# Optimization experiments

Hardware: AMD Instinct MI355X
Metric: run time of the kernel (lower is better)

Reference implementation:

```python
import jax, jax.numpy as jnp
import numpy as np

KNOW = 128
EXER_N = 20000
STU_N = 50000
N_EDGES = 1000000
N_EDGES_P = 950000
BATCH = 8192
SOFT_PARA = 0.2
EPS = 1e-8


def setup_inputs() -> dict:
    key = jax.random.key(0)
    ks = jax.random.split(key, 10)
    return {
        'stu_emb': jax.random.normal(ks[0], (STU_N, KNOW), jnp.float32) * 0.1,
        'exer_emb': jax.random.normal(ks[1], (EXER_N, KNOW), jnp.float32) * 0.1,
        'W_ue': jax.random.normal(ks[2], (KNOW, KNOW), jnp.float32) / np.sqrt(KNOW),
        'W_ue_per': jax.random.normal(ks[3], (KNOW, KNOW), jnp.float32) / np.sqrt(KNOW),
        'W_deep': jax.random.normal(ks[4], (KNOW, KNOW), jnp.float32) / np.sqrt(KNOW),
        'src_e': jax.random.randint(ks[5], (N_EDGES,), 0, EXER_N),
        'dst_e': jax.random.randint(ks[6], (N_EDGES,), 0, STU_N),
        'src_p': jax.random.randint(ks[7], (N_EDGES_P,), 0, EXER_N),
        'dst_p': jax.random.randint(ks[8], (N_EDGES_P,), 0, STU_N),
        'stu_id': jax.random.randint(ks[9], (BATCH,), 0, STU_N),
    }


def _graph_layer(exer, W, src, dst):
    # u_from_e: messages flow exercise -> student. Linear transform then mean-aggregate.
    msg = exer[src] @ W                                   # [E_edges, K]
    agg = jax.ops.segment_sum(msg, dst, num_segments=STU_N)
    deg = jax.ops.segment_sum(jnp.ones_like(dst, jnp.float32), dst, num_segments=STU_N)
    return agg / jnp.maximum(deg, 1.0)[:, None]           # [STU_N, K]


def reference(stu_emb, exer_emb, W_ue, W_ue_per, W_deep, src_e, dst_e, src_p, dst_p, stu_id):
    # ExpressionDooubleEva: two parallel graph views
    stu1 = stu_emb + _graph_layer(exer_emb, W_ue, src_e, dst_e)
    stu_per = stu_emb + _graph_layer(exer_emb, W_ue_per, src_p, dst_p)
    # ExpressionSingleEva (u_from_e output is overwritten by u_from_e_deep in source)
    stu2 = stu1 + _graph_layer(exer_emb, W_deep, src_e, dst_e)
    stu2_per = stu_per + _graph_layer(exer_emb, W_deep, src_e, dst_e)

    b1 = stu2[stu_id]          # [B, K]
    b2 = stu2_per[stu_id]      # [B, K]
    n1 = b1 / jnp.linalg.norm(b1, axis=1, keepdims=True)
    n2 = b2 / jnp.linalg.norm(b2, axis=1, keepdims=True)
    sim = (n1 @ n2.T) / SOFT_PARA                         # [B, B]
    # faithful to source: numerator = exp(diag(sim)), denominator = sum of RAW sim row
    diag_exp = jnp.exp(jnp.diagonal(sim))
    row_sum = jnp.sum(sim, axis=1)
    ratio = diag_exp / (row_sum + EPS)
    ssl_loss = jnp.mean(-jnp.log(jnp.maximum(ratio, EPS)))
    return stu2, ssl_loss
```

## Files before the change

kernel.cpp:

```cpp
#include <hip/hip_runtime.h>
#include <math.h>

#define KNOW 128
#define STU_N 50000
#define EXER_N 20000
#define BATCH 8192
#define NE 1000000
#define NEP 950000
#define SOFT_INV 5.0f
#define EPS 1e-8f

#define CAP 64
#define NBIN 256
#define SPB 196
#define SSE 4608
#define SSP 1536
#define P1B 256
#define P1T 512
#define SFB 32
#define WPB 24
#define TFB 250
#define BM_T 80

typedef unsigned short u16;
typedef unsigned int u32;

typedef __attribute__((ext_vector_type(8))) short bf16x8;
typedef __attribute__((ext_vector_type(4))) float f32x4;

__device__ __forceinline__ u16 f2bf(float f) {
  union { float f; u32 u; } v;
  v.f = f;
  u32 r = (v.u + 0x7FFFu + ((v.u >> 16) & 1u)) >> 16;
  return (u16)r;
}
__device__ __forceinline__ float bflo(u32 u) {
  union { u32 u; float f; } v;
  v.u = u << 16;
  return v.f;
}
__device__ __forceinline__ float bfhi(u32 u) {
  union { u32 u; float f; } v;
  v.u = u & 0xFFFF0000u;
  return v.f;
}
__device__ __forceinline__ float bfu(u16 h) {
  union { u32 u; float f; } v;
  v.u = ((u32)h) << 16;
  return v.f;
}

#define ADD8(A, q)            \
  {                           \
    A[0] += bflo((q).x);      \
    A[1] += bfhi((q).x);      \
    A[2] += bflo((q).y);      \
    A[3] += bfhi((q).y);      \
    A[4] += bflo((q).z);      \
    A[5] += bfhi((q).z);      \
    A[6] += bflo((q).w);      \
    A[7] += bfhi((q).w);      \
  }

__global__ __launch_bounds__(256) void prep_flags(
    const int* __restrict__ stu_id, unsigned char* __restrict__ flag,
    int* __restrict__ gcur_e, int* __restrict__ gcur_p,
    const float* __restrict__ exer, const float* __restrict__ W_ue,
    const float* __restrict__ W_per, const float* __restrict__ W_deep,
    u16* __restrict__ Ah, u16* __restrict__ Al, u16* __restrict__ WTh,
    u16* __restrict__ WTl) {
  int b = blockIdx.x;
  int t = threadIdx.x;
  if (b < SFB) {
    int i = b * 256 + t;
    if (i < BATCH) flag[stu_id[i]] = 1;
    if (i < NBIN) {
      gcur_e[i] = i * SSE;
      gcur_p[i] = i * SSP;
    }
  } else if (b < SFB + WPB) {
    int plane = (b - SFB) >> 3;
    int slab = (b - SFB) & 7;
    int n = t & 127;
    int k0 = slab * 16 + (t >> 7) * 8;
    const float* W0 = (plane == 0) ? W_ue : (plane == 1) ? W_per : W_deep;
    float x[8];
#pragma unroll
    for (int j = 0; j < 8; ++j) {
      float v = W0[(k0 + j) * KNOW + n];
      if (plane == 0) v += W_deep[(k0 + j) * KNOW + n];
      x[j] = v;
    }
    u16 hi[8], lo[8];
#pragma unroll
    for (int j = 0; j < 8; ++j) {
      u16 h = f2bf(x[j]);
      hi[j] = h;
      lo[j] = f2bf(x[j] - bfu(h));
    }
    size_t base = ((size_t)plane * KNOW + n) * KNOW + k0;
    uint4 H = {(u32)hi[0] | ((u32)hi[1] << 16), (u32)hi[2] | ((u32)hi[3] << 16),
               (u32)hi[4] | ((u32)hi[5] << 16), (u32)hi[6] | ((u32)hi[7] << 16)};
    uint4 L = {(u32)lo[0] | ((u32)lo[1] << 16), (u32)lo[2] | ((u32)lo[3] << 16),
               (u32)lo[4] | ((u32)lo[5] << 16), (u32)lo[6] | ((u32)lo[7] << 16)};
    *(uint4*)(WTh + base) = H;
    *(uint4*)(WTl + base) = L;
  } else {
    size_t i = ((size_t)(b - SFB - WPB) * 256 + t) * 4;
    float4 v = *(const float4*)(exer + i);
    u16 h0 = f2bf(v.x), h1 = f2bf(v.y), h2 = f2bf(v.z), h3 = f2bf(v.w);
    ushort4 H = {h0, h1, h2, h3};
    ushort4 L = {f2bf(v.x - bfu(h0)), f2bf(v.y - bfu(h1)), f2bf(v.z - bfu(h2)),
                 f2bf(v.w - bfu(h3))};
    *(ushort4*)(Ah + i) = H;
    *(ushort4*)(Al + i) = L;
  }
}

__global__ __launch_bounds__(P1T) void transform_bin1(
    const u16* __restrict__ Ah, const u16* __restrict__ Al,
    const u16* __restrict__ WTh, const u16* __restrict__ WTl,
    u16* __restrict__ X_sum, u16* __restrict__ X_per,
    u16* __restrict__ X_deep, const int* __restrict__ dst_e,
    const int* __restrict__ src_e, const int* __restrict__ dst_p,
    const int* __restrict__ src_p, const unsigned char* __restrict__ flag,
    int* __restrict__ gcur_e, int* __restrict__ gcur_p,
    u32* __restrict__ stag_e, u32* __restrict__ stag_p) {
  __shared__ int cntE[NBIN], cntP[NBIN];
  __shared__ int baseE[NBIN], baseP[NBIN];
  __shared__ int curE[NBIN], curP[NBIN];
  int t = threadIdx.x;
  if (blockIdx.x < P1B) {
    if (t < NBIN) {
      cntE[t] = 0;
      cntP[t] = 0;
    }
    __syncthreads();
    int b = blockIdx.x;
    int e0 = (int)((long long)NE * b / P1B);
    int e1 = (int)((long long)NE * (b + 1) / P1B);
    int p0 = (int)((long long)NEP * b / P1B);
    int p1 = (int)((long long)NEP * (b + 1) / P1B);
    for (int i = e0 + t; i < e1; i += P1T) {
      int d = __builtin_nontemporal_load(&dst_e[i]);
      atomicAdd(&cntE[d / SPB], 1);
    }
    for (int i = p0 + t; i < p1; i += P1T) {
      int d = __builtin_nontemporal_load(&dst_p[i]);
      if (flag[d]) atomicAdd(&cntP[d / SPB], 1);
    }
    __syncthreads();
    if (t < NBIN) {
      baseE[t] = atomicAdd(&gcur_e[t], cntE[t]);
      baseP[t] = atomicAdd(&gcur_p[t], cntP[t]);
      curE[t] = 0;
      curP[t] = 0;
    }
    __syncthreads();
    for (int i = e0 + t; i < e1; i += P1T) {
      int d = __builtin_nontemporal_load(&dst_e[i]);
      int s = __builtin_nontemporal_load(&src_e[i]);
      int bin = d / SPB;
      int pos = baseE[bin] + atomicAdd(&curE[bin], 1);
      if (pos < (bin + 1) * SSE)
        stag_e[pos] = ((u32)(d - bin * SPB) << 16) | (u32)s;
    }
    for (int i = p0 + t; i < p1; i += P1T) {
      int d = __builtin_nontemporal_load(&dst_p[i]);
      if (!flag[d]) continue;
      int s = __builtin_nontemporal_load(&src_p[i]);
      int bin = d / SPB;
      int pos = baseP[bin] + atomicAdd(&curP[bin], 1);
      if (pos < (bin + 1) * SSP)
        stag_p[pos] = ((u32)(d - bin * SPB) << 16) | (u32)s;
    }
  } else {
    int wv = t >> 6;
    int l = t & 63;
    int bn = l & 15;
    int kb = l >> 4;
    int row0 = (blockIdx.x - P1B) * BM_T;
    int n = wv * 16 + bn;
#pragma unroll 1
    for (int which = 0; which < 3; ++which) {
      u16* outp = (which == 0) ? X_sum : (which == 1) ? X_per : X_deep;
      const u16* wth = WTh + (size_t)which * KNOW * KNOW;
      const u16* wtl = WTl + (size_t)which * KNOW * KNOW;
      bf16x8 bh[4], bl[4];
#pragma unroll
      for (int ks = 0; ks < 4; ++ks) {
        int off = n * KNOW + ks * 32 + kb * 8;
        bh[ks] = *(const bf16x8*)(wth + off);
        bl[ks] = *(const bf16x8*)(wtl + off);
      }
#pragma unroll 1
      for (int rt = 0; rt < 5; ++rt) {
        int row = row0 + rt * 16 + bn;
        const u16* ap = Ah + (size_t)row * KNOW + kb * 8;
        const u16* alp = Al + (size_t)row * KNOW + kb * 8;
        f32x4 acc = {0.f, 0.f, 0.f, 0.f};
#pragma unroll
        for (int ks = 0; ks < 4; ++ks) {
          bf16x8 af = *(const bf16x8*)(ap + ks * 32);
          bf16x8 lf = *(const bf16x8*)(alp + ks * 32);
          acc = __builtin_amdgcn_mfma_f32_16x16x32_bf16(af, bh[ks], acc, 0, 0, 0);
          acc = __builtin_amdgcn_mfma_f32_16x16x32_bf16(lf, bh[ks], acc, 0, 0, 0);
          acc = __builtin_amdgcn_mfma_f32_16x16x32_bf16(af, bl[ks], acc, 0, 0, 0);
        }
        int orow = row0 + rt * 16 + kb * 4;
#pragma unroll
        for (int r = 0; r < 4; ++r)
          outp[(size_t)(orow + r) * KNOW + n] = f2bf(acc[r]);
      }
    }
  }
}

__global__ __launch_bounds__(256) void bin_pass2(
    const u32* __restrict__ stag_e, const u32* __restrict__ stag_p,
    const int* __restrict__ gcur_e, const int* __restrict__ gcur_p,
    u16* __restrict__ bucket_e, u16* __restrict__ bucket_p,
    int* __restrict__ cnt_e, int* __restrict__ cnt_p) {
  __shared__ u16 be[SPB * CAP];
  __shared__ u16 bp[SPB * CAP];
  __shared__ int ce[SPB], cp[SPB];
  int t = threadIdx.x;
  int bin = blockIdx.x;
  for (int i = t; i < SPB; i += 256) {
    ce[i] = 0;
    cp[i] = 0;
  }
  __syncthreads();
  int ne = gcur_e[bin] - bin * SSE;
  if (ne > SSE) ne = SSE;
  int np = gcur_p[bin] - bin * SSP;
  if (np > SSP) np = SSP;
  const u32* se = stag_e + (size_t)bin * SSE;
  for (int i = t; i < ne; i += 256) {
    u32 w = se[i];
    int dl = (int)(w >> 16), s = (int)(w & 0xFFFFu);
    int slot = atomicAdd(&ce[dl], 1);
    if (slot < CAP) be[dl * CAP + slot] = (u16)s;
  }
  const u32* sp = stag_p + (size_t)bin * SSP;
  for (int i = t; i < np; i += 256) {
    u32 w = sp[i];
    int dl = (int)(w >> 16), s = (int)(w & 0xFFFFu);
    int slot = atomicAdd(&cp[dl], 1);
    if (slot < CAP) bp[dl * CAP + slot] = (u16)s;
  }
  __syncthreads();
  int s0 = bin * SPB;
  int nstu = STU_N - s0;
  if (nstu > SPB) nstu = SPB;
  if (nstu <= 0) return;
  int nvec = nstu * CAP * 2 / 16;
  const uint4* bev = (const uint4*)be;
  uint4* ge = (uint4*)(bucket_e + (size_t)s0 * CAP);
  for (int i = t; i < nvec; i += 256) ge[i] = bev[i];
  const uint4* bpv = (const uint4*)bp;
  uint4* gp = (uint4*)(bucket_p + (size_t)s0 * CAP);
  for (int i = t; i < nvec; i += 256) gp[i] = bpv[i];
  for (int i = t; i < nstu; i += 256) {
    cnt_e[s0 + i] = ce[i];
    cnt_p[s0 + i] = cp[i];
  }
}

__global__ __launch_bounds__(256) void stu2_gather(
    const float* __restrict__ stu_emb, const u16* __restrict__ X_sum,
    const u16* __restrict__ bucket, const int* __restrict__ cnt,
    float* __restrict__ out) {
  int wv = threadIdx.x >> 6;
  int l = threadIdx.x & 63;
  int s = blockIdx.x * 4 + wv;
  if (s >= STU_N) return;
  int deg = cnt[s];
  int e = (deg < CAP) ? deg : CAP;
  u32 bval = bucket[(size_t)s * CAP + l];
  int g = l >> 4;
  int c = l & 15;
  float acc[8] = {};
  for (int i = g; i < e; i += 16) {
    int iB = i + 4, iC = i + 8, iD = i + 12;
    int jB = (iB < e) ? iB : i;
    int jC = (iC < e) ? iC : i;
    int jD = (iD < e) ? iD : i;
    int rA = __shfl((int)bval, i);
    int rB = __shfl((int)bval, jB);
    int rC = __shfl((int)bval, jC);
    int rD = __shfl((int)bval, jD);
    const uint4 qA = *(const uint4*)(X_sum + (size_t)rA * KNOW + c * 8);
    const uint4 qB = *(const uint4*)(X_sum + (size_t)rB * KNOW + c * 8);
    const uint4 qC = *(const uint4*)(X_sum + (size_t)rC * KNOW + c * 8);
    const uint4 qD = *(const uint4*)(X_sum + (size_t)rD * KNOW + c * 8);
    ADD8(acc, qA);
    if (iB < e) ADD8(acc, qB);
    if (iC < e) ADD8(acc, qC);
    if (iD < e) ADD8(acc, qD);
  }
#pragma unroll
  for (int j = 0; j < 8; ++j) {
    float v = acc[j];
    v += __shfl_xor(v, 16);
    v += __shfl_xor(v, 32);
    acc[j] = v;
  }
  if (l < 16) {
    float inv = 1.0f / fmaxf((float)deg, 1.0f);
    float4 se0 = *(const float4*)(stu_emb + (size_t)s * KNOW + c * 8);
    float4 se1 = *(const float4*)(stu_emb + (size_t)s * KNOW + c * 8 + 4);
    float4 o0 = {se0.x + acc[0] * inv, se0.y + acc[1] * inv,
                 se0.z + acc[2] * inv, se0.w + acc[3] * inv};
    float4 o1 = {se1.x + acc[4] * inv, se1.y + acc[5] * inv,
                 se1.z + acc[6] * inv, se1.w + acc[7] * inv};
    *(float4*)(out + (size_t)s * KNOW + c * 8) = o0;
    *(float4*)(out + (size_t)s * KNOW + c * 8 + 4) = o1;
  }
}

__global__ __launch_bounds__(256) void batch_kernel(
    const float* __restrict__ stu_emb, const float* __restrict__ stu2,
    const u16* __restrict__ X_per, const u16* __restrict__ X_deep,
    const u16* __restrict__ bucket_p, const int* __restrict__ cnt_p,
    const u16* __restrict__ bucket_e, const int* __restrict__ cnt_e,
    const int* __restrict__ stu_id, float* __restrict__ n1,
    float* __restrict__ n2, float* __restrict__ diag) {
  int wv = threadIdx.x >> 6;
  int l = threadIdx.x & 63;
  int i = blockIdx.x * 4 + wv;
  int sid = stu_id[i];
  int g = l >> 4;
  int c = l & 15;

  int degp = cnt_p[sid];
  int degd = cnt_e[sid];
  u32 bvp = bucket_p[(size_t)sid * CAP + l];
  u32 bvd = bucket_e[(size_t)sid * CAP + l];
  int ep = (degp < CAP) ? degp : CAP;
  int ed = (degd < CAP) ? degd : CAP;

  float ap[8] = {};
  for (int t = g; t < ep; t += 16) {
    int iB = t + 4, iC = t + 8, iD = t + 12;
    int jB = (iB < ep) ? iB : t;
    int jC = (iC < ep) ? iC : t;
    int jD = (iD < ep) ? iD : t;
    int rA = __shfl((int)bvp, t);
    int rB = __shfl((int)bvp, jB);
    int rC = __shfl((int)bvp, jC);
    int rD = __shfl((int)bvp, jD);
    const uint4 qA = *(const uint4*)(X_per + (size_t)rA * KNOW + c * 8);
    const uint4 qB = *(const uint4*)(X_per + (size_t)rB * KNOW + c * 8);
    const uint4 qC = *(const uint4*)(X_per + (size_t)rC * KNOW + c * 8);
    const uint4 qD = *(const uint4*)(X_per + (size_t)rD * KNOW + c * 8);
    ADD8(ap, qA);
    if (iB < ep) ADD8(ap, qB);
    if (iC < ep) ADD8(ap, qC);
    if (iD < ep) ADD8(ap, qD);
  }

  float ad[8] = {};
  for (int t = g; t < ed; t += 16) {
    int iB = t + 4, iC = t + 8, iD = t + 12;
    int jB = (iB < ed) ? iB : t;
    int jC = (iC < ed) ? iC : t;
    int jD = (iD < ed) ? iD : t;
    int rA = __shfl((int)bvd, t);
    int rB = __shfl((int)bvd, jB);
    int rC = __shfl((int)bvd, jC);
    int rD = __shfl((int)bvd, jD);
    const uint4 qA = *(const uint4*)(X_deep + (size_t)rA * KNOW + c * 8);
    const uint4 qB = *(const uint4*)(X_deep + (size_t)rB * KNOW + c * 8);
    const uint4 qC = *(const uint4*)(X_deep + (size_t)rC * KNOW + c * 8);
    const uint4 qD = *(const uint4*)(X_deep + (size_t)rD * KNOW + c * 8);
    ADD8(ad, qA);
    if (iB < ed) ADD8(ad, qB);
    if (iC < ed) ADD8(ad, qC);
    if (iD < ed) ADD8(ad, qD);
  }

#pragma unroll
  for (int j = 0; j < 8; ++j) {
    float v = ap[j];
    v += __shfl_xor(v, 16);
    v += __shfl_xor(v, 32);
    ap[j] = v;
    float w = ad[j];
    w += __shfl_xor(w, 16);
    w += __shfl_xor(w, 32);
    ad[j] = w;
  }

  float invp = 1.0f / fmaxf((float)degp, 1.0f);
  float invd = 1.0f / fmaxf((float)degd, 1.0f);
  float4 e0 = *(const float4*)(stu_emb + (size_t)sid * KNOW + c * 8);
  float4 e1 = *(const float4*)(stu_emb + (size_t)sid * KNOW + c * 8 + 4);
  float4 s0 = *(const float4*)(stu2 + (size_t)sid * KNOW + c * 8);
  float4 s1 = *(const float4*)(stu2 + (size_t)sid * KNOW + c * 8 + 4);
  float b1v[8] = {s0.x, s0.y, s0.z, s0.w, s1.x, s1.y, s1.z, s1.w};
  float ev[8] = {e0.x, e0.y, e0.z, e0.w, e1.x, e1.y, e1.z, e1.w};
  float b2v[8];
  float s11 = 0.f, s22 = 0.f, s12 = 0.f;
#pragma unroll
  for (int j = 0; j < 8; ++j) {
    b2v[j] = ev[j] + ap[j] * invp + ad[j] * invd;
    s11 += b1v[j] * b1v[j];
    s22 += b2v[j] * b2v[j];
    s12 += b1v[j] * b2v[j];
  }
#pragma unroll
  for (int off = 1; off <= 8; off <<= 1) {
    s11 += __shfl_xor(s11, off);
    s22 += __shfl_xor(s22, off);
    s12 += __shfl_xor(s12, off);
  }
  float norm1 = sqrtf(s11);
  float norm2 = sqrtf(s22);
  if (g == 0) {
    float4 o0 = {b1v[0] / norm1, b1v[1] / norm1, b1v[2] / norm1,
                 b1v[3] / norm1};
    float4 o1 = {b1v[4] / norm1, b1v[5] / norm1, b1v[6] / norm1,
                 b1v[7] / norm1};
    *(float4*)(n1 + (size_t)i * KNOW + c * 8) = o0;
    *(float4*)(n1 + (size_t)i * KNOW + c * 8 + 4) = o1;
  } else if (g == 1) {
    float4 o0 = {b2v[0] / norm2, b2v[1] / norm2, b2v[2] / norm2,
                 b2v[3] / norm2};
    float4 o1 = {b2v[4] / norm2, b2v[5] / norm2, b2v[6] / norm2,
                 b2v[7] / norm2};
    *(float4*)(n2 + (size_t)i * KNOW + c * 8) = o0;
    *(float4*)(n2 + (size_t)i * KNOW + c * 8 + 4) = o1;
  } else if (g == 2 && c == 0) {
    diag[i] = s12 / (norm1 * norm2);
  }
}

__global__ __launch_bounds__(128) void s2_reduce(const float* __restrict__ n2,
                                                 float* __restrict__ S2) {
  int k = threadIdx.x;
  int r0 = blockIdx.x * (BATCH / 64);
  float acc = 0.0f;
  for (int r = 0; r < BATCH / 64; ++r) acc += n2[(size_t)(r0 + r) * KNOW + k];
  atomicAdd(&S2[k], acc);
}

#define L2BLKS 64
__global__ __launch_bounds__(256) void loss2_fin(
    const float* __restrict__ n1, const float* __restrict__ diag,
    const float* __restrict__ S2, float* __restrict__ loss,
    int* __restrict__ done, float* __restrict__ out) {
  __shared__ float s2s[KNOW];
  int t = threadIdx.x;
  if (t < KNOW) s2s[t] = S2[t];
  __syncthreads();
  int wave = t >> 6, lane = t & 63;
  const int rows_per_wave = BATCH / (L2BLKS * 4);
  int r0 = (blockIdx.x * 4 + wave) * rows_per_wave;
  float acc = 0.0f;
  for (int r = r0; r < r0 + rows_per_wave; ++r) {
    float v = n1[(size_t)r * KNOW + lane] * s2s[lane] +
              n1[(size_t)r * KNOW + 64 + lane] * s2s[64 + lane];
#pragma unroll
    for (int off = 32; off > 0; off >>= 1) v += __shfl_down(v, off);
    if (lane == 0) {
      float rs = v * SOFT_INV;
      float dg = diag[r] * SOFT_INV;
      float ratio = expf(dg) / (rs + EPS);
      acc += -logf(fmaxf(ratio, EPS));
    }
  }
  if (lane == 0) atomicAdd(loss, acc);
  __syncthreads();
  if (t == 0) {
    __threadfence();
    int old = atomicAdd(done, 1);
    if (old == L2BLKS - 1) {
      float total = atomicAdd(loss, 0.0f);
      out[(size_t)STU_N * KNOW] = total * (1.0f / (float)BATCH);
    }
  }
}

extern "C" void kernel_launch(void* const* d_in, const int* in_sizes, int n_in,
                              void* d_out, int out_size, void* d_ws,
                              size_t ws_size, hipStream_t stream) {
  const float* stu_emb = (const float*)d_in[0];
  const float* exer_emb = (const float*)d_in[1];
  const float* W_ue = (const float*)d_in[2];
  const float* W_ue_per = (const float*)d_in[3];
  const float* W_deep = (const float*)d_in[4];
  const int* src_e = (const int*)d_in[5];
  const int* dst_e = (const int*)d_in[6];
  const int* src_p = (const int*)d_in[7];
  const int* dst_p = (const int*)d_in[8];
  const int* stu_id = (const int*)d_in[9];
  float* out = (float*)d_out;

  char* wsb = (char*)d_ws;
  float* S2 = (float*)wsb;
  float* loss = S2 + KNOW;
  int* done = (int*)(loss + 1);
  unsigned char* flag = (unsigned char*)(done + 1);
  size_t zero_bytes = (size_t)((char*)flag + STU_N - wsb);
  char* rest = wsb + ((zero_bytes + 63) & ~(size_t)63);
  int* cnt_e = (int*)rest;
  int* cnt_p = cnt_e + STU_N;
  int* gcur_e = cnt_p + STU_N;
  int* gcur_p = gcur_e + NBIN;
  u16* X_sum = (u16*)(gcur_p + NBIN);
  u16* X_per = X_sum + (size_t)EXER_N * KNOW;
  u16* X_deep = X_per + (size_t)EXER_N * KNOW;
  u16* bucket_e = X_deep + (size_t)EXER_N * KNOW;
  u16* bucket_p = bucket_e + (size_t)STU_N * CAP;
  u32* stag_e = (u32*)(bucket_p + (size_t)STU_N * CAP);
  u32* stag_p = stag_e + (size_t)NBIN * SSE;
  float* n1 = (float*)(stag_p + (size_t)NBIN * SSP);
  float* n2 = n1 + (size_t)BATCH * KNOW;
  float* diag = n2 + (size_t)BATCH * KNOW;
  u16* Ah = (u16*)(diag + BATCH);
  u16* Al = Ah + (size_t)EXER_N * KNOW;
  u16* WTh = Al + (size_t)EXER_N * KNOW;
  u16* WTl = WTh + (size_t)3 * KNOW * KNOW;

  hipMemsetAsync(d_ws, 0, zero_bytes, stream);

  prep_flags<<<SFB + WPB + EXER_N * KNOW / 1024, 256, 0, stream>>>(
      stu_id, flag, gcur_e, gcur_p, exer_emb, W_ue, W_ue_per, W_deep, Ah, Al,
      WTh, WTl);

  transform_bin1<<<P1B + TFB, P1T, 0, stream>>>(
      Ah, Al, WTh, WTl, X_sum, X_per, X_deep, dst_e, src_e, dst_p, src_p, flag,
      gcur_e, gcur_p, stag_e, stag_p);

  bin_pass2<<<NBIN, 256, 0, stream>>>(stag_e, stag_p, gcur_e, gcur_p, bucket_e,
                                      bucket_p, cnt_e, cnt_p);

  stu2_gather<<<(STU_N + 3) / 4, 256, 0, stream>>>(stu_emb, X_sum, bucket_e,
                                                   cnt_e, out);

  batch_kernel<<<BATCH / 4, 256, 0, stream>>>(stu_emb, out, X_per, X_deep,
                                              bucket_p, cnt_p, bucket_e, cnt_e,
                                              stu_id, n1, n2, diag);

  s2_reduce<<<64, 128, 0, stream>>>(n2, S2);

  loss2_fin<<<L2BLKS, 256, 0, stream>>>(n1, diag, S2, loss, done, out);
}
```

Measured before the change: 254.9 us.

## Merge full-student gather and batch gather into one kernel launch

Fuses the stu2 gather and the batch kernel into a single launch. Batch blocks come first and no longer read stu2 from the first kernel's output; they recompute b1 themselves by also gathering X_sum over the e-graph neighbours, which removes the dependency between the two phases. The aim is to drop one launch and the serialization gap so both phases overlap on the GPU, at the cost of extra X_sum gather traffic for the batch rows.

```diff
diff --git a/kernel.cpp b/kernel.cpp
--- a/kernel.cpp
+++ b/kernel.cpp
@@ -21,6 +21,8 @@
 #define WPB 24
 #define TFB 250
 #define BM_T 80
+#define BATCHB (BATCH / 4)
+#define STU2B ((STU_N + 3) / 4)
 
 typedef unsigned short u16;
 typedef unsigned int u32;
@@ -267,72 +269,67 @@
   }
 }
 
-__global__ __launch_bounds__(256) void stu2_gather(
+__global__ __launch_bounds__(256) void gather_all(
     const float* __restrict__ stu_emb, const u16* __restrict__ X_sum,
-    const u16* __restrict__ bucket, const int* __restrict__ cnt,
-    float* __restrict__ out) {
+    const u16* __restrict__ X_per, const u16* __restrict__ X_deep,
+    const u16* __restrict__ bucket_e, const int* __restrict__ cnt_e,
+    const u16* __restrict__ bucket_p, const int* __restrict__ cnt_p,
+    const int* __restrict__ stu_id, float* __restrict__ out,
+    float* __restrict__ n1, float* __restrict__ n2,
+    float* __restrict__ diag) {
   int wv = threadIdx.x >> 6;
   int l = threadIdx.x & 63;
-  int s = blockIdx.x * 4 + wv;
-  if (s >= STU_N) return;
-  int deg = cnt[s];
-  int e = (deg < CAP) ? deg : CAP;
-  u32 bval = bucket[(size_t)s * CAP + l];
   int g = l >> 4;
   int c = l & 15;
-  float acc[8] = {};
-  for (int i = g; i < e; i += 16) {
-    int iB = i + 4, iC = i + 8, iD = i + 12;
-    int jB = (iB < e) ? iB : i;
-    int jC = (iC < e) ? iC : i;
-    int jD = (iD < e) ? iD : i;
-    int rA = __shfl((int)bval, i);
-    int rB = __shfl((int)bval, jB);
-    int rC = __shfl((int)bval, jC);
-    int rD = __shfl((int)bval, jD);
-    const uint4 qA = *(const uint4*)(X_sum + (size_t)rA * KNOW + c * 8);
-    const uint4 qB = *(const uint4*)(X_sum + (size_t)rB * KNOW + c * 8);
-    const uint4 qC = *(const uint4*)(X_sum + (size_t)rC * KNOW + c * 8);
-    const uint4 qD = *(const uint4*)(X_sum + (size_t)rD * KNOW + c * 8);
-    ADD8(acc, qA);
-    if (iB < e) ADD8(acc, qB);
-    if (iC < e) ADD8(acc, qC);
-    if (iD < e) ADD8(acc, qD);
-  }
-#pragma unroll
-  for (int j = 0; j < 8; ++j) {
-    float v = acc[j];
-    v += __shfl_xor(v, 16);
-    v += __shfl_xor(v, 32);
-    acc[j] = v;
-  }
-  if (l < 16) {
-    float inv = 1.0f / fmaxf((float)deg, 1.0f);
-    float4 se0 = *(const float4*)(stu_emb + (size_t)s * KNOW + c * 8);
-    float4 se1 = *(const float4*)(stu_emb + (size_t)s * KNOW + c * 8 + 4);
-    float4 o0 = {se0.x + acc[0] * inv, se0.y + acc[1] * inv,
-                 se0.z + acc[2] * inv, se0.w + acc[3] * inv};
-    float4 o1 = {se1.x + acc[4] * inv, se1.y + acc[5] * inv,
-                 se1.z + acc[6] * inv, se1.w + acc[7] * inv};
-    *(float4*)(out + (size_t)s * KNOW + c * 8) = o0;
-    *(float4*)(out + (size_t)s * KNOW + c * 8 + 4) = o1;
-  }
-}
-
-__global__ __launch_bounds__(256) void batch_kernel(
-    const float* __restrict__ stu_emb, const float* __restrict__ stu2,
-    const u16* __restrict__ X_per, const u16* __restrict__ X_deep,
-    const u16* __restrict__ bucket_p, const int* __restrict__ cnt_p,
-    const u16* __restrict__ bucket_e, const int* __restrict__ cnt_e,
-    const int* __restrict__ stu_id, float* __restrict__ n1,
-    float* __restrict__ n2, float* __restrict__ diag) {
-  int wv = threadIdx.x >> 6;
-  int l = threadIdx.x & 63;
+
+  if (blockIdx.x >= BATCHB) {
+    int s = (blockIdx.x - BATCHB) * 4 + wv;
+    if (s >= STU_N) return;
+    int deg = cnt_e[s];
+    int e = (deg < CAP) ? deg : CAP;
+    u32 bval = bucket_e[(size_t)s * CAP + l];
+    float acc[8] = {};
+    for (int i = g; i < e; i += 16) {
+      int iB = i + 4, iC = i + 8, iD = i + 12;
+      int jB = (iB < e) ? iB : i;
+      int jC = (iC < e) ? iC : i;
+      int jD = (iD < e) ? iD : i;
+      int rA = __shfl((int)bval, i);
+      int rB = __shfl((int)bval, jB);
+      int rC = __shfl((int)bval, jC);
+      int rD = __shfl((int)bval, jD);
+      const uint4 qA = *(const uint4*)(X_sum + (size_t)rA * KNOW + c * 8);
+      const uint4 qB = *(const uint4*)(X_sum + (size_t)rB * KNOW + c * 8);
+      const uint4 qC = *(const uint4*)(X_sum + (size_t)rC * KNOW + c * 8);
+      const uint4 qD = *(const uint4*)(X_sum + (size_t)rD * KNOW + c * 8);
+      ADD8(acc, qA);
+      if (iB < e) ADD8(acc, qB);
+      if (iC < e) ADD8(acc, qC);
+      if (iD < e) ADD8(acc, qD);
+    }
+#pragma unroll
+    for (int j = 0; j < 8; ++j) {
+      float v = acc[j];
+      v += __shfl_xor(v, 16);
+      v += __shfl_xor(v, 32);
+      acc[j] = v;
+    }
+    if (l < 16) {
+      float inv = 1.0f / fmaxf((float)deg, 1.0f);
+      float4 se0 = *(const float4*)(stu_emb + (size_t)s * KNOW + c * 8);
+      float4 se1 = *(const float4*)(stu_emb + (size_t)s * KNOW + c * 8 + 4);
+      float4 o0 = {se0.x + acc[0] * inv, se0.y + acc[1] * inv,
+                   se0.z + acc[2] * inv, se0.w + acc[3] * inv};
+      float4 o1 = {se1.x + acc[4] * inv, se1.y + acc[5] * inv,
+                   se1.z + acc[6] * inv, se1.w + acc[7] * inv};
+      *(float4*)(out + (size_t)s * KNOW + c * 8) = o0;
+      *(float4*)(out + (size_t)s * KNOW + c * 8 + 4) = o1;
+    }
+    return;
+  }
+
   int i = blockIdx.x * 4 + wv;
   int sid = stu_id[i];
-  int g = l >> 4;
-  int c = l & 15;
-
   int degp = cnt_p[sid];
   int degd = cnt_e[sid];
   u32 bvp = bucket_p[(size_t)sid * CAP + l];
@@ -360,7 +357,7 @@
     if (iD < ep) ADD8(ap, qD);
   }
 
-  float ad[8] = {};
+  float ad[8] = {}, as_[8] = {};
   for (int t = g; t < ed; t += 16) {
     int iB = t + 4, iC = t + 8, iD = t + 12;
     int jB = (iB < ed) ? iB : t;
@@ -370,14 +367,28 @@
     int rB = __shfl((int)bvd, jB);
     int rC = __shfl((int)bvd, jC);
     int rD = __shfl((int)bvd, jD);
-    const uint4 qA = *(const uint4*)(X_deep + (size_t)rA * KNOW + c * 8);
-    const uint4 qB = *(const uint4*)(X_deep + (size_t)rB * KNOW + c * 8);
-    const uint4 qC = *(const uint4*)(X_deep + (size_t)rC * KNOW + c * 8);
-    const uint4 qD = *(const uint4*)(X_deep + (size_t)rD * KNOW + c * 8);
-    ADD8(ad, qA);
-    if (iB < ed) ADD8(ad, qB);
-    if (iC < ed) ADD8(ad, qC);
-    if (iD < ed) ADD8(ad, qD);
+    const uint4 dA = *(const uint4*)(X_deep + (size_t)rA * KNOW + c * 8);
+    const uint4 sA = *(const uint4*)(X_sum + (size_t)rA * KNOW + c * 8);
+    const uint4 dB = *(const uint4*)(X_deep + (size_t)rB * KNOW + c * 8);
+    const uint4 sB = *(const uint4*)(X_sum + (size_t)rB * KNOW + c * 8);
+    const uint4 dC = *(const uint4*)(X_deep + (size_t)rC * KNOW + c * 8);
+    const uint4 sC = *(const uint4*)(X_sum + (size_t)rC * KNOW + c * 8);
+    const uint4 dD = *(const uint4*)(X_deep + (size_t)rD * KNOW + c * 8);
+    const uint4 sD = *(const uint4*)(X_sum + (size_t)rD * KNOW + c * 8);
+    ADD8(ad, dA);
+    ADD8(as_, sA);
+    if (iB < ed) {
+      ADD8(ad, dB);
+      ADD8(as_, sB);
+    }
+    if (iC < ed) {
+      ADD8(ad, dC);
+      ADD8(as_, sC);
+    }
+    if (iD < ed) {
+      ADD8(ad, dD);
+      ADD8(as_, sD);
+    }
   }
 
 #pragma unroll
@@ -390,20 +401,22 @@
     w += __shfl_xor(w, 16);
     w += __shfl_xor(w, 32);
     ad[j] = w;
+    float u = as_[j];
+    u += __shfl_xor(u, 16);
+    u += __shfl_xor(u, 32);
+    as_[j] = u;
   }
 
   float invp = 1.0f / fmaxf((float)degp, 1.0f);
   float invd = 1.0f / fmaxf((float)degd, 1.0f);
   float4 e0 = *(const float4*)(stu_emb + (size_t)sid * KNOW + c * 8);
   float4 e1 = *(const float4*)(stu_emb + (size_t)sid * KNOW + c * 8 + 4);
-  float4 s0 = *(const float4*)(stu2 + (size_t)sid * KNOW + c * 8);
-  float4 s1 = *(const float4*)(stu2 + (size_t)sid * KNOW + c * 8 + 4);
-  float b1v[8] = {s0.x, s0.y, s0.z, s0.w, s1.x, s1.y, s1.z, s1.w};
   float ev[8] = {e0.x, e0.y, e0.z, e0.w, e1.x, e1.y, e1.z, e1.w};
-  float b2v[8];
+  float b1v[8], b2v[8];
   float s11 = 0.f, s22 = 0.f, s12 = 0.f;
 #pragma unroll
   for (int j = 0; j < 8; ++j) {
+    b1v[j] = ev[j] + as_[j] * invd;
     b2v[j] = ev[j] + ap[j] * invp + ad[j] * invd;
     s11 += b1v[j] * b1v[j];
     s22 += b2v[j] * b2v[j];
@@ -536,12 +549,9 @@
   bin_pass2<<<NBIN, 256, 0, stream>>>(stag_e, stag_p, gcur_e, gcur_p, bucket_e,
                                       bucket_p, cnt_e, cnt_p);
 
-  stu2_gather<<<(STU_N + 3) / 4, 256, 0, stream>>>(stu_emb, X_sum, bucket_e,
-                                                   cnt_e, out);
-
-  batch_kernel<<<BATCH / 4, 256, 0, stream>>>(stu_emb, out, X_per, X_deep,
-                                              bucket_p, cnt_p, bucket_e, cnt_e,
-                                              stu_id, n1, n2, diag);
+  gather_all<<<BATCHB + STU2B, 256, 0, stream>>>(
+      stu_emb, X_sum, X_per, X_deep, bucket_e, cnt_e, bucket_p, cnt_p, stu_id,
+      out, n1, n2, diag);
 
   s2_reduce<<<64, 128, 0, stream>>>(n2, S2);
 
```

New measurement: 260.8 us. 2.3% more time.
